# Kernel tuning notes

Hardware: AMD Instinct MI355X
Metric: run time of the kernel (lower is better)

The kernel has to match this reference:

```python
import jax, jax.numpy as jnp
import numpy as np

N_TOKENS = 32768
DIM = 2048
N_EXPERTS = 64
TOP_K = 8
N_GROUP = 8
TOPK_GROUP = 4
ROUTE_SCALE = 2.5
EPS = 1e-20


def setup_inputs() -> dict:
    key = jax.random.key(0)
    k1, k2 = jax.random.split(key)
    hidden_states = jax.random.normal(k1, (N_TOKENS, DIM), dtype=jnp.float32)
    weight = jax.random.normal(k2, (N_EXPERTS, DIM), dtype=jnp.float32) * 0.02
    e_score_correction_bias = jnp.zeros((N_EXPERTS,), dtype=jnp.float32)
    return {"hidden_states": hidden_states, "weight": weight,
            "e_score_correction_bias": e_score_correction_bias}


def reference(hidden_states, weight, e_score_correction_bias):
    # router logits in fp32: [N, E]
    logits = jnp.einsum('nd,ed->ne', hidden_states.astype(jnp.float32),
                        weight.astype(jnp.float32))
    scores = jax.nn.sigmoid(logits)  # score_func == 'sigmoid'

    # --- top-k index selection (no-grad path in torch) ---
    sfc = scores + e_score_correction_bias[None, :]  # [N, E]
    per_group = N_EXPERTS // N_GROUP
    # group score = sum of top-2 scores within each group: [N, G]
    grouped = sfc.reshape(-1, N_GROUP, per_group)
    group_scores = jax.lax.top_k(grouped, 2)[0].sum(axis=-1)
    # pick top `TOPK_GROUP` groups
    _, group_idx = jax.lax.top_k(group_scores, TOPK_GROUP)  # [N, topk_group]
    n = group_scores.shape[0]
    group_mask = jnp.zeros_like(group_scores).at[
        jnp.arange(n)[:, None], group_idx].set(1.0)  # [N, G]
    score_mask = jnp.repeat(group_mask, per_group, axis=1)  # [N, E]
    masked_scores = jnp.where(score_mask > 0, sfc, 0.0)
    _, topk_indices = jax.lax.top_k(masked_scores, TOP_K)  # [N, top_k]

    # gather weights from *unbiased* scores, normalize, scale
    topk_weights = jnp.take_along_axis(scores, topk_indices, axis=1)
    denom = topk_weights.sum(axis=-1, keepdims=True) + EPS
    topk_weights = topk_weights / denom * ROUTE_SCALE
    return topk_indices, topk_weights
```

## Files before the change

### kernel.cpp

```cpp
#include <hip/hip_runtime.h>
#include <math.h>

#define NT 32768
#define DIM 2048
#define NE 64
#define RSCALE 2.5f
#define REPS 1e-20f
#define KC 32
#define NCH (DIM / KC)
#define TOK 64

#define HL_BUF 12288
#define WL_OFF 24576
#define BS_OFF 49152
#define ARENA 49408

typedef __attribute__((ext_vector_type(8))) short short8x;
typedef __attribute__((ext_vector_type(4))) float f32x4;
typedef __attribute__((ext_vector_type(4))) unsigned int uint4x;

#define PACKHI(odd, even) __builtin_amdgcn_perm((odd), (even), 0x07060302u)

__device__ __forceinline__ void decomp4(f32x4 x, unsigned int o[6]) {
    unsigned int u0 = __float_as_uint(x.x), u1 = __float_as_uint(x.y);
    unsigned int u2 = __float_as_uint(x.z), u3 = __float_as_uint(x.w);
    o[0] = PACKHI(u1, u0); o[1] = PACKHI(u3, u2);
    float r0 = x.x - __uint_as_float(u0 & 0xffff0000u);
    float r1 = x.y - __uint_as_float(u1 & 0xffff0000u);
    float r2 = x.z - __uint_as_float(u2 & 0xffff0000u);
    float r3 = x.w - __uint_as_float(u3 & 0xffff0000u);
    unsigned int v0 = __float_as_uint(r0), v1 = __float_as_uint(r1);
    unsigned int v2 = __float_as_uint(r2), v3 = __float_as_uint(r3);
    o[2] = PACKHI(v1, v0); o[3] = PACKHI(v3, v2);
    float s0 = r0 - __uint_as_float(v0 & 0xffff0000u);
    float s1 = r1 - __uint_as_float(v1 & 0xffff0000u);
    float s2 = r2 - __uint_as_float(v2 & 0xffff0000u);
    float s3 = r3 - __uint_as_float(v3 & 0xffff0000u);
    o[4] = PACKHI(__float_as_uint(s1), __float_as_uint(s0));
    o[5] = PACKHI(__float_as_uint(s3), __float_as_uint(s2));
}

__device__ __forceinline__ void decomp8(f32x4 a, f32x4 b,
                                        short8x* f0, short8x* f1, short8x* f2) {
    unsigned int oa[6], ob[6];
    decomp4(a, oa); decomp4(b, ob);
    uint4x t0 = {oa[0], oa[1], ob[0], ob[1]};
    uint4x t1 = {oa[2], oa[3], ob[2], ob[3]};
    uint4x t2 = {oa[4], oa[5], ob[4], ob[5]};
    *f0 = __builtin_bit_cast(short8x, t0);
    *f1 = __builtin_bit_cast(short8x, t1);
    *f2 = __builtin_bit_cast(short8x, t2);
}

#define BARRIER() do { \
    asm volatile("s_waitcnt lgkmcnt(0)" ::: "memory"); \
    __builtin_amdgcn_s_barrier(); \
    __builtin_amdgcn_sched_barrier(0); \
} while (0)

#define STAGE_ISSUE(HA, HB, WA, WB, KOFF) do { \
    HA = *(const f32x4*)(hgsrc + (KOFF));     \
    HB = *(const f32x4*)(hgsrc + (KOFF) + 4); \
    WA = *(const f32x4*)(wgsrc + (KOFF));     \
    WB = *(const f32x4*)(wgsrc + (KOFF) + 4); \
} while (0)

#define STAGE_WRITE(HA, HB, WA, WB, PN) do { \
    short8x f0_, f1_, f2_; \
    decomp8(HA, HB, &f0_, &f1_, &f2_); \
    *(short8x*)(arena + (PN) * HL_BUF + 0 * 4096 + soff) = f0_; \
    *(short8x*)(arena + (PN) * HL_BUF + 1 * 4096 + soff) = f1_; \
    *(short8x*)(arena + (PN) * HL_BUF + 2 * 4096 + soff) = f2_; \
    decomp8(WA, WB, &f0_, &f1_, &f2_); \
    *(short8x*)(arena + WL_OFF + (PN) * HL_BUF + 0 * 4096 + soff) = f0_; \
    *(short8x*)(arena + WL_OFF + (PN) * HL_BUF + 1 * 4096 + soff) = f1_; \
    *(short8x*)(arena + WL_OFF + (PN) * HL_BUF + 2 * 4096 + soff) = f2_; \
} while (0)

#define COMPUTE(P) do { \
    const char* hb = arena + (P) * HL_BUF; \
    const char* wb = arena + WL_OFF + (P) * HL_BUF; \
    short8x a0[2], a1[2], a2[2]; \
    _Pragma("unroll") \
    for (int tt = 0; tt < 2; ++tt) { \
        const int t_ = wr * 32 + tt * 16 + l15; \
        const int ro_ = t_ * 64 + ((g ^ ((t_ >> 1) & 3)) << 4); \
        a0[tt] = *(const short8x*)(hb + 0 * 4096 + ro_); \
        a1[tt] = *(const short8x*)(hb + 1 * 4096 + ro_); \
        a2[tt] = *(const short8x*)(hb + 2 * 4096 + ro_); \
    } \
    _Pragma("unroll") \
    for (int et = 0; et < 2; ++et) { \
        const int e_ = wc * 32 + et * 16 + l15; \
        const int ro_ = e_ * 64 + ((g ^ ((e_ >> 1) & 3)) << 4); \
        short8x b0 = *(const short8x*)(wb + 0 * 4096 + ro_); \
        short8x b1 = *(const short8x*)(wb + 1 * 4096 + ro_); \
        short8x b2 = *(const short8x*)(wb + 2 * 4096 + ro_); \
        _Pragma("unroll") \
        for (int tt = 0; tt < 2; ++tt) { \
            Cm[tt][et] = __builtin_amdgcn_mfma_f32_16x16x32_bf16(a0[tt], b0, Cm[tt][et], 0, 0, 0); \
            Cc[tt][et] = __builtin_amdgcn_mfma_f32_16x16x32_bf16(a1[tt], b0, Cc[tt][et], 0, 0, 0); \
            Cc[tt][et] = __builtin_amdgcn_mfma_f32_16x16x32_bf16(a2[tt], b0, Cc[tt][et], 0, 0, 0); \
            Cc[tt][et] = __builtin_amdgcn_mfma_f32_16x16x32_bf16(a0[tt], b1, Cc[tt][et], 0, 0, 0); \
            Cc[tt][et] = __builtin_amdgcn_mfma_f32_16x16x32_bf16(a1[tt], b1, Cc[tt][et], 0, 0, 0); \
            Cc[tt][et] = __builtin_amdgcn_mfma_f32_16x16x32_bf16(a0[tt], b2, Cc[tt][et], 0, 0, 0); \
        } \
    } \
} while (0)

#define DRAIN do { \
    _Pragma("unroll") \
    for (int tt = 0; tt < 2; ++tt) \
        _Pragma("unroll") \
        for (int et = 0; et < 2; ++et) { \
            _Pragma("unroll") \
            for (int r = 0; r < 4; ++r) \
                md[tt][et][r] += (double)Cm[tt][et][r] + (double)Cc[tt][et][r]; \
            Cm[tt][et] = (f32x4)0.0f; Cc[tt][et] = (f32x4)0.0f; \
        } \
} while (0)

__global__ __launch_bounds__(256, 2) void router_kernel(
    const float* __restrict__ H,
    const float* __restrict__ W,
    const float* __restrict__ B,
    float* __restrict__ out)
{
    __shared__ __align__(16) char arena[ARENA];
    float* bsf = (float*)(arena + BS_OFF);
    float* scf = (float*)(arena);

    const int tid  = threadIdx.x;
    const int lane = tid & 63;
    const int w    = __builtin_amdgcn_readfirstlane(tid >> 6);
    const int l15  = lane & 15, g = lane >> 4;
    const size_t tb = (size_t)blockIdx.x * TOK;

    if (tid < NE) bsf[tid] = B[tid];

    const int srow = tid >> 2;
    const int sq   = tid & 3;
    const float* hgsrc = H + (tb + (size_t)srow) * DIM + sq * 8;
    const float* wgsrc = W + (size_t)srow * DIM + sq * 8;
    const int soff = srow * 64 + ((sq ^ ((srow >> 1) & 3)) << 4);

    const int wr = w & 1, wc = w >> 1;

    f32x4 Cm[2][2], Cc[2][2];
    double md[2][2][4];
    #pragma unroll
    for (int tt = 0; tt < 2; ++tt)
        #pragma unroll
        for (int et = 0; et < 2; ++et) {
            Cm[tt][et] = (f32x4)0.0f; Cc[tt][et] = (f32x4)0.0f;
            #pragma unroll
            for (int r = 0; r < 4; ++r) md[tt][et][r] = 0.0;
        }

    f32x4 hA0, hA1, wA0, wA1, hB0, hB1, wB0, wB1;

    STAGE_ISSUE(hA0, hA1, wA0, wA1, 0);
    STAGE_WRITE(hA0, hA1, wA0, wA1, 0);
    STAGE_ISSUE(hB0, hB1, wB0, wB1, KC);
    BARRIER();

    for (int chb = 0; chb < NCH; chb += 2) {
        if (chb + 2 < NCH) STAGE_ISSUE(hA0, hA1, wA0, wA1, (chb + 2) * KC);
        COMPUTE(0);
        STAGE_WRITE(hB0, hB1, wB0, wB1, 1);
        BARRIER();

        if (chb + 3 < NCH) STAGE_ISSUE(hB0, hB1, wB0, wB1, (chb + 3) * KC);
        COMPUTE(1);
        if (chb + 2 < NCH) STAGE_WRITE(hA0, hA1, wA0, wA1, 0);
        if (((chb + 1) & 7) == 7) DRAIN;
        BARRIER();
    }

    #pragma unroll
    for (int tt = 0; tt < 2; ++tt)
        #pragma unroll
        for (int et = 0; et < 2; ++et)
            #pragma unroll
            for (int r = 0; r < 4; ++r) {
                float logit = (float)md[tt][et][r];
                float s = 1.0f / (1.0f + expf(-logit));
                int t = wr * 32 + tt * 16 + g * 4 + r;
                int e = wc * 32 + et * 16 + l15;
                scf[t * 65 + e] = s;
            }
    __syncthreads();

    if ((tid & 3) == 0) {
        const int t = tid >> 2;
        const float* sc = &scf[t * 65];
        float gs[8];
        #pragma unroll
        for (int gg = 0; gg < 8; ++gg) {
            float m1 = -1e30f, m2 = -1e30f;
            #pragma unroll
            for (int j = 0; j < 8; ++j) {
                float v = sc[gg * 8 + j] + bsf[gg * 8 + j];
                if (v > m1) { m2 = m1; m1 = v; }
                else if (v > m2) { m2 = v; }
            }
            gs[gg] = m1 + m2;
        }
        unsigned gmask = 0;
        for (int i = 0; i < 4; ++i) {
            float best = -1e30f; int bg = 0;
            for (int gg = 0; gg < 8; ++gg)
                if (!((gmask >> gg) & 1u) && gs[gg] > best) { best = gs[gg]; bg = gg; }
            gmask |= 1u << bg;
        }
        unsigned long long picked = 0ull;
        int   idxs[8];
        float wts[8];
        float wsum = 0.0f;
        for (int i = 0; i < 8; ++i) {
            float best = -1e30f; int bi = 0;
            for (int e = 0; e < 64; ++e) {
                if ((picked >> e) & 1ull) continue;
                float v = ((gmask >> (e >> 3)) & 1u) ? (sc[e] + bsf[e]) : 0.0f;
                if (v > best) { best = v; bi = e; }
            }
            picked |= 1ull << bi;
            idxs[i] = bi;
            wts[i] = sc[bi];
            wsum += sc[bi];
        }
        const float scale = RSCALE / (wsum + REPS);
        const size_t token = tb + t;
        #pragma unroll
        for (int i = 0; i < 8; ++i) {
            out[token * 8 + i] = (float)idxs[i];
            out[(size_t)NT * 8 + token * 8 + i] = wts[i] * scale;
        }
    }
}

extern "C" void kernel_launch(void* const* d_in, const int* in_sizes, int n_in,
                              void* d_out, int out_size, void* d_ws, size_t ws_size,
                              hipStream_t stream) {
    (void)in_sizes; (void)n_in; (void)out_size; (void)d_ws; (void)ws_size;
    const float* H = (const float*)d_in[0];
    const float* W = (const float*)d_in[1];
    const float* B = (const float*)d_in[2];
    float* out = (float*)d_out;
    router_kernel<<<dim3(NT / TOK), dim3(256), 0, stream>>>(H, W, B, out);
}
```

Baseline: 131.7 us.

## Split router GEMM along K into four slices with separate top-k reduction kernel

Splits the fp32-emulated GEMM over the hidden dimension into four K-slices on a second grid axis. Partial double-precision logits go to a global scratch buffer, and a new kernel sums them before applying sigmoid and group top-k. Shared memory drops to a single staging buffer with extra barriers so more blocks fit per CU (launch bounds raised to 5). The cost is a 64MB double round trip through global memory, a second kernel launch, and less overlap between loads and compute.

```diff
diff --git a/kernel.cpp b/kernel.cpp
--- a/kernel.cpp
+++ b/kernel.cpp
@@ -7,17 +7,19 @@
 #define RSCALE 2.5f
 #define REPS 1e-20f
 #define KC 32
-#define NCH (DIM / KC)
+#define NSPLIT 4
+#define KSEG (DIM / NSPLIT)
+#define NCHB (KSEG / KC)
 #define TOK 64
 
-#define HL_BUF 12288
-#define WL_OFF 24576
-#define BS_OFF 49152
-#define ARENA 49408
+#define WL_OFF 12288
+#define ARENA 24576
 
 typedef __attribute__((ext_vector_type(8))) short short8x;
 typedef __attribute__((ext_vector_type(4))) float f32x4;
 typedef __attribute__((ext_vector_type(4))) unsigned int uint4x;
+
+__device__ double wsbuf[NSPLIT][NT][NE];
 
 #define PACKHI(odd, even) __builtin_amdgcn_perm((odd), (even), 0x07060302u)
 
@@ -65,21 +67,21 @@
     WB = *(const f32x4*)(wgsrc + (KOFF) + 4); \
 } while (0)
 
-#define STAGE_WRITE(HA, HB, WA, WB, PN) do { \
+#define STAGE_WRITE(HA, HB, WA, WB) do { \
     short8x f0_, f1_, f2_; \
     decomp8(HA, HB, &f0_, &f1_, &f2_); \
-    *(short8x*)(arena + (PN) * HL_BUF + 0 * 4096 + soff) = f0_; \
-    *(short8x*)(arena + (PN) * HL_BUF + 1 * 4096 + soff) = f1_; \
-    *(short8x*)(arena + (PN) * HL_BUF + 2 * 4096 + soff) = f2_; \
+    *(short8x*)(arena + 0 * 4096 + soff) = f0_; \
+    *(short8x*)(arena + 1 * 4096 + soff) = f1_; \
+    *(short8x*)(arena + 2 * 4096 + soff) = f2_; \
     decomp8(WA, WB, &f0_, &f1_, &f2_); \
-    *(short8x*)(arena + WL_OFF + (PN) * HL_BUF + 0 * 4096 + soff) = f0_; \
-    *(short8x*)(arena + WL_OFF + (PN) * HL_BUF + 1 * 4096 + soff) = f1_; \
-    *(short8x*)(arena + WL_OFF + (PN) * HL_BUF + 2 * 4096 + soff) = f2_; \
-} while (0)
-
-#define COMPUTE(P) do { \
-    const char* hb = arena + (P) * HL_BUF; \
-    const char* wb = arena + WL_OFF + (P) * HL_BUF; \
+    *(short8x*)(arena + WL_OFF + 0 * 4096 + soff) = f0_; \
+    *(short8x*)(arena + WL_OFF + 1 * 4096 + soff) = f1_; \
+    *(short8x*)(arena + WL_OFF + 2 * 4096 + soff) = f2_; \
+} while (0)
+
+#define COMPUTE() do { \
+    const char* hb = arena; \
+    const char* wb = arena + WL_OFF; \
     short8x a0[2], a1[2], a2[2]; \
     _Pragma("unroll") \
     for (int tt = 0; tt < 2; ++tt) { \
@@ -120,28 +122,24 @@
         } \
 } while (0)
 
-__global__ __launch_bounds__(256, 2) void router_kernel(
+__global__ __launch_bounds__(256, 5) void router_gemm(
     const float* __restrict__ H,
-    const float* __restrict__ W,
-    const float* __restrict__ B,
-    float* __restrict__ out)
+    const float* __restrict__ W)
 {
     __shared__ __align__(16) char arena[ARENA];
-    float* bsf = (float*)(arena + BS_OFF);
-    float* scf = (float*)(arena);
 
     const int tid  = threadIdx.x;
     const int lane = tid & 63;
     const int w    = __builtin_amdgcn_readfirstlane(tid >> 6);
     const int l15  = lane & 15, g = lane >> 4;
     const size_t tb = (size_t)blockIdx.x * TOK;
-
-    if (tid < NE) bsf[tid] = B[tid];
+    const int split = blockIdx.y;
+    const int kbase = split * KSEG;
 
     const int srow = tid >> 2;
     const int sq   = tid & 3;
-    const float* hgsrc = H + (tb + (size_t)srow) * DIM + sq * 8;
-    const float* wgsrc = W + (size_t)srow * DIM + sq * 8;
+    const float* hgsrc = H + (tb + (size_t)srow) * DIM + kbase + sq * 8;
+    const float* wgsrc = W + (size_t)srow * DIM + kbase + sq * 8;
     const int soff = srow * 64 + ((sq ^ ((srow >> 1) & 3)) << 4);
 
     const int wr = w & 1, wc = w >> 1;
@@ -160,20 +158,22 @@
     f32x4 hA0, hA1, wA0, wA1, hB0, hB1, wB0, wB1;
 
     STAGE_ISSUE(hA0, hA1, wA0, wA1, 0);
-    STAGE_WRITE(hA0, hA1, wA0, wA1, 0);
     STAGE_ISSUE(hB0, hB1, wB0, wB1, KC);
+    STAGE_WRITE(hA0, hA1, wA0, wA1);
     BARRIER();
 
-    for (int chb = 0; chb < NCH; chb += 2) {
-        if (chb + 2 < NCH) STAGE_ISSUE(hA0, hA1, wA0, wA1, (chb + 2) * KC);
-        COMPUTE(0);
-        STAGE_WRITE(hB0, hB1, wB0, wB1, 1);
-        BARRIER();
-
-        if (chb + 3 < NCH) STAGE_ISSUE(hB0, hB1, wB0, wB1, (chb + 3) * KC);
-        COMPUTE(1);
-        if (chb + 2 < NCH) STAGE_WRITE(hA0, hA1, wA0, wA1, 0);
+    for (int chb = 0; chb < NCHB; chb += 2) {
+        COMPUTE();
+        if (chb + 2 < NCHB) STAGE_ISSUE(hA0, hA1, wA0, wA1, (chb + 2) * KC);
+        BARRIER();
+        STAGE_WRITE(hB0, hB1, wB0, wB1);
+        BARRIER();
+
+        COMPUTE();
+        if (chb + 3 < NCHB) STAGE_ISSUE(hB0, hB1, wB0, wB1, (chb + 3) * KC);
         if (((chb + 1) & 7) == 7) DRAIN;
+        BARRIER();
+        if (chb + 2 < NCHB) STAGE_WRITE(hA0, hA1, wA0, wA1);
         BARRIER();
     }
 
@@ -182,13 +182,33 @@
         #pragma unroll
         for (int et = 0; et < 2; ++et)
             #pragma unroll
-            for (int r = 0; r < 4; ++r) {
-                float logit = (float)md[tt][et][r];
-                float s = 1.0f / (1.0f + expf(-logit));
-                int t = wr * 32 + tt * 16 + g * 4 + r;
-                int e = wc * 32 + et * 16 + l15;
-                scf[t * 65 + e] = s;
-            }
+            for (int r = 0; r < 4; ++r)
+                wsbuf[split][tb + wr * 32 + tt * 16 + g * 4 + r]
+                     [wc * 32 + et * 16 + l15] = md[tt][et][r];
+}
+
+__global__ __launch_bounds__(256) void router_topk(
+    const float* __restrict__ B,
+    float* __restrict__ out)
+{
+    __shared__ float scf[TOK * 65];
+    __shared__ float bsf[NE];
+
+    const int tid = threadIdx.x;
+    const size_t tb = (size_t)blockIdx.x * TOK;
+
+    if (tid < NE) bsf[tid] = B[tid];
+
+    const int e  = tid & 63;
+    const int t4 = tid >> 6;
+    #pragma unroll
+    for (int pass = 0; pass < 16; ++pass) {
+        const int t = pass * 4 + t4;
+        const size_t token = tb + t;
+        double m = ((wsbuf[0][token][e] + wsbuf[1][token][e])
+                  + wsbuf[2][token][e]) + wsbuf[3][token][e];
+        scf[t * 65 + e] = 1.0f / (1.0f + expf(-(float)m));
+    }
     __syncthreads();
 
     if ((tid & 3) == 0) {
@@ -219,10 +239,10 @@
         float wsum = 0.0f;
         for (int i = 0; i < 8; ++i) {
             float best = -1e30f; int bi = 0;
-            for (int e = 0; e < 64; ++e) {
-                if ((picked >> e) & 1ull) continue;
-                float v = ((gmask >> (e >> 3)) & 1u) ? (sc[e] + bsf[e]) : 0.0f;
-                if (v > best) { best = v; bi = e; }
+            for (int ee = 0; ee < 64; ++ee) {
+                if ((picked >> ee) & 1ull) continue;
+                float v = ((gmask >> (ee >> 3)) & 1u) ? (sc[ee] + bsf[ee]) : 0.0f;
+                if (v > best) { best = v; bi = ee; }
             }
             picked |= 1ull << bi;
             idxs[i] = bi;
@@ -247,5 +267,6 @@
     const float* W = (const float*)d_in[1];
     const float* B = (const float*)d_in[2];
     float* out = (float*)d_out;
-    router_kernel<<<dim3(NT / TOK), dim3(256), 0, stream>>>(H, W, B, out);
-}
+    router_gemm<<<dim3(NT / TOK, NSPLIT), dim3(256), 0, stream>>>(H, W);
+    router_topk<<<dim3(NT / TOK), dim3(256), 0, stream>>>(B, out);
+}
```

Result: slower. 294.6 us (+123.7%).

## Split K across two wave groups per block with LDS reduction of partial logits

Applied to the files above, without the earlier changes.

Doubles the block to 512 threads, split into two 4-wave groups. Each group handles half of the DIM reduction with its own single-buffered LDS staging area, and the double-precision partial sums are combined through shared memory before the sigmoid and top-k step. The aim is more waves in flight per CU to hide global load latency, and a shorter serial K loop per wave. In exchange the per-group double buffering becomes a single buffer with extra barriers, and a reduction pass through LDS is added.

```diff
diff --git a/kernel.cpp b/kernel.cpp
--- a/kernel.cpp
+++ b/kernel.cpp
@@ -7,13 +7,16 @@
 #define RSCALE 2.5f
 #define REPS 1e-20f
 #define KC 32
-#define NCH (DIM / KC)
+#define NCHG 32
+#define KSEG (NCHG * KC)
 #define TOK 64
 
-#define HL_BUF 12288
-#define WL_OFF 24576
-#define BS_OFF 49152
-#define ARENA 49408
+#define GRP_ARENA 24576
+#define WL_OFF 12288
+#define MD_OFF 0
+#define SC_OFF 32768
+#define BS_OFF 49408
+#define ARENA 49664
 
 typedef __attribute__((ext_vector_type(8))) short short8x;
 typedef __attribute__((ext_vector_type(4))) float f32x4;
@@ -65,21 +68,21 @@
     WB = *(const f32x4*)(wgsrc + (KOFF) + 4); \
 } while (0)
 
-#define STAGE_WRITE(HA, HB, WA, WB, PN) do { \
+#define STAGE_WRITE(HA, HB, WA, WB) do { \
     short8x f0_, f1_, f2_; \
     decomp8(HA, HB, &f0_, &f1_, &f2_); \
-    *(short8x*)(arena + (PN) * HL_BUF + 0 * 4096 + soff) = f0_; \
-    *(short8x*)(arena + (PN) * HL_BUF + 1 * 4096 + soff) = f1_; \
-    *(short8x*)(arena + (PN) * HL_BUF + 2 * 4096 + soff) = f2_; \
+    *(short8x*)(ga + 0 * 4096 + soff) = f0_; \
+    *(short8x*)(ga + 1 * 4096 + soff) = f1_; \
+    *(short8x*)(ga + 2 * 4096 + soff) = f2_; \
     decomp8(WA, WB, &f0_, &f1_, &f2_); \
-    *(short8x*)(arena + WL_OFF + (PN) * HL_BUF + 0 * 4096 + soff) = f0_; \
-    *(short8x*)(arena + WL_OFF + (PN) * HL_BUF + 1 * 4096 + soff) = f1_; \
-    *(short8x*)(arena + WL_OFF + (PN) * HL_BUF + 2 * 4096 + soff) = f2_; \
-} while (0)
-
-#define COMPUTE(P) do { \
-    const char* hb = arena + (P) * HL_BUF; \
-    const char* wb = arena + WL_OFF + (P) * HL_BUF; \
+    *(short8x*)(ga + WL_OFF + 0 * 4096 + soff) = f0_; \
+    *(short8x*)(ga + WL_OFF + 1 * 4096 + soff) = f1_; \
+    *(short8x*)(ga + WL_OFF + 2 * 4096 + soff) = f2_; \
+} while (0)
+
+#define COMPUTE() do { \
+    const char* hb = ga; \
+    const char* wb = ga + WL_OFF; \
     short8x a0[2], a1[2], a2[2]; \
     _Pragma("unroll") \
     for (int tt = 0; tt < 2; ++tt) { \
@@ -120,7 +123,7 @@
         } \
 } while (0)
 
-__global__ __launch_bounds__(256, 2) void router_kernel(
+__global__ __launch_bounds__(512, 4) void router_kernel(
     const float* __restrict__ H,
     const float* __restrict__ W,
     const float* __restrict__ B,
@@ -128,23 +131,30 @@
 {
     __shared__ __align__(16) char arena[ARENA];
     float* bsf = (float*)(arena + BS_OFF);
-    float* scf = (float*)(arena);
+    float* scf = (float*)(arena + SC_OFF);
+    double* mdb = (double*)(arena + MD_OFF);
 
     const int tid  = threadIdx.x;
     const int lane = tid & 63;
     const int w    = __builtin_amdgcn_readfirstlane(tid >> 6);
+    const int grp  = w >> 2;
+    const int wl   = w & 3;
     const int l15  = lane & 15, g = lane >> 4;
     const size_t tb = (size_t)blockIdx.x * TOK;
+    const int kbase = grp * KSEG;
+
+    char* ga = arena + grp * GRP_ARENA;
 
     if (tid < NE) bsf[tid] = B[tid];
 
-    const int srow = tid >> 2;
-    const int sq   = tid & 3;
-    const float* hgsrc = H + (tb + (size_t)srow) * DIM + sq * 8;
-    const float* wgsrc = W + (size_t)srow * DIM + sq * 8;
+    const int gtid = tid & 255;
+    const int srow = gtid >> 2;
+    const int sq   = gtid & 3;
+    const float* hgsrc = H + (tb + (size_t)srow) * DIM + kbase + sq * 8;
+    const float* wgsrc = W + (size_t)srow * DIM + kbase + sq * 8;
     const int soff = srow * 64 + ((sq ^ ((srow >> 1) & 3)) << 4);
 
-    const int wr = w & 1, wc = w >> 1;
+    const int wr = wl & 1, wc = wl >> 1;
 
     f32x4 Cm[2][2], Cc[2][2];
     double md[2][2][4];
@@ -160,38 +170,53 @@
     f32x4 hA0, hA1, wA0, wA1, hB0, hB1, wB0, wB1;
 
     STAGE_ISSUE(hA0, hA1, wA0, wA1, 0);
-    STAGE_WRITE(hA0, hA1, wA0, wA1, 0);
     STAGE_ISSUE(hB0, hB1, wB0, wB1, KC);
+    STAGE_WRITE(hA0, hA1, wA0, wA1);
     BARRIER();
 
-    for (int chb = 0; chb < NCH; chb += 2) {
-        if (chb + 2 < NCH) STAGE_ISSUE(hA0, hA1, wA0, wA1, (chb + 2) * KC);
-        COMPUTE(0);
-        STAGE_WRITE(hB0, hB1, wB0, wB1, 1);
-        BARRIER();
-
-        if (chb + 3 < NCH) STAGE_ISSUE(hB0, hB1, wB0, wB1, (chb + 3) * KC);
-        COMPUTE(1);
-        if (chb + 2 < NCH) STAGE_WRITE(hA0, hA1, wA0, wA1, 0);
+    for (int chb = 0; chb < NCHG; chb += 2) {
+        COMPUTE();
+        if (chb + 2 < NCHG) STAGE_ISSUE(hA0, hA1, wA0, wA1, (chb + 2) * KC);
+        BARRIER();
+        STAGE_WRITE(hB0, hB1, wB0, wB1);
+        BARRIER();
+
+        COMPUTE();
+        if (chb + 3 < NCHG) STAGE_ISSUE(hB0, hB1, wB0, wB1, (chb + 3) * KC);
         if (((chb + 1) & 7) == 7) DRAIN;
         BARRIER();
-    }
-
-    #pragma unroll
-    for (int tt = 0; tt < 2; ++tt)
-        #pragma unroll
-        for (int et = 0; et < 2; ++et)
-            #pragma unroll
-            for (int r = 0; r < 4; ++r) {
-                float logit = (float)md[tt][et][r];
-                float s = 1.0f / (1.0f + expf(-logit));
-                int t = wr * 32 + tt * 16 + g * 4 + r;
-                int e = wc * 32 + et * 16 + l15;
-                scf[t * 65 + e] = s;
-            }
+        if (chb + 2 < NCHG) STAGE_WRITE(hA0, hA1, wA0, wA1);
+        BARRIER();
+    }
+
+    if (grp == 1) {
+        #pragma unroll
+        for (int tt = 0; tt < 2; ++tt)
+            #pragma unroll
+            for (int et = 0; et < 2; ++et)
+                #pragma unroll
+                for (int r = 0; r < 4; ++r)
+                    mdb[((tt * 2 + et) * 4 + r) * 256 + gtid] = md[tt][et][r];
+    }
     __syncthreads();
 
-    if ((tid & 3) == 0) {
+    if (grp == 0) {
+        #pragma unroll
+        for (int tt = 0; tt < 2; ++tt)
+            #pragma unroll
+            for (int et = 0; et < 2; ++et)
+                #pragma unroll
+                for (int r = 0; r < 4; ++r) {
+                    double m = md[tt][et][r] + mdb[((tt * 2 + et) * 4 + r) * 256 + gtid];
+                    float s = 1.0f / (1.0f + expf(-(float)m));
+                    int t = wr * 32 + tt * 16 + g * 4 + r;
+                    int e = wc * 32 + et * 16 + l15;
+                    scf[t * 65 + e] = s;
+                }
+    }
+    __syncthreads();
+
+    if (tid < 256 && (tid & 3) == 0) {
         const int t = tid >> 2;
         const float* sc = &scf[t * 65];
         float gs[8];
@@ -247,5 +272,5 @@
     const float* W = (const float*)d_in[1];
     const float* B = (const float*)d_in[2];
     float* out = (float*)d_out;
-    router_kernel<<<dim3(NT / TOK), dim3(256), 0, stream>>>(H, W, B, out);
-}
+    router_kernel<<<dim3(NT / TOK), dim3(512), 0, stream>>>(H, W, B, out);
+}
```

New measurement: 155.3 us. +17.9%, slower.

## Precompute bf16-split weight image and stream it to LDS with direct loads

Applied to the files above, without the earlier changes.

Adds a prep kernel that converts the router weight into its three-way bf16 split form once, laid out in the swizzled LDS layout, and stores it in a global buffer. The main kernel then copies weight tiles straight into LDS with global_load_lds instead of loading fp32 weights and decomposing them in every block. This removes redundant per-block weight conversion and register traffic. In exchange it adds a second kernel launch, triples the weight bytes read per chunk, and replaces the custom barrier with __syncthreads, which waits on outstanding memory counters.

```diff
diff --git a/kernel.cpp b/kernel.cpp
--- a/kernel.cpp
+++ b/kernel.cpp
@@ -15,9 +15,13 @@
 #define BS_OFF 49152
 #define ARENA 49408
 
+typedef const __attribute__((address_space(1))) void GV;
+typedef __attribute__((address_space(3))) void LV;
 typedef __attribute__((ext_vector_type(8))) short short8x;
 typedef __attribute__((ext_vector_type(4))) float f32x4;
 typedef __attribute__((ext_vector_type(4))) unsigned int uint4x;
+
+__device__ __align__(16) char WImg[NCH][3 * 4096];
 
 #define PACKHI(odd, even) __builtin_amdgcn_perm((odd), (even), 0x07060302u)
 
@@ -52,29 +56,43 @@
     *f2 = __builtin_bit_cast(short8x, t2);
 }
 
-#define BARRIER() do { \
-    asm volatile("s_waitcnt lgkmcnt(0)" ::: "memory"); \
-    __builtin_amdgcn_s_barrier(); \
-    __builtin_amdgcn_sched_barrier(0); \
-} while (0)
-
-#define STAGE_ISSUE(HA, HB, WA, WB, KOFF) do { \
-    HA = *(const f32x4*)(hgsrc + (KOFF));     \
+__global__ void prep_w_kernel(const float* __restrict__ W) {
+    const int ch = blockIdx.x;
+    const int tid = threadIdx.x;
+    const int srow = tid >> 2;
+    const int sq   = tid & 3;
+    const float* src = W + (size_t)srow * DIM + ch * KC + sq * 8;
+    f32x4 lo = *(const f32x4*)src;
+    f32x4 hi = *(const f32x4*)(src + 4);
+    short8x f0, f1, f2;
+    decomp8(lo, hi, &f0, &f1, &f2);
+    const int soff = srow * 64 + ((sq ^ ((srow >> 1) & 3)) << 4);
+    *(short8x*)&WImg[ch][0 * 4096 + soff] = f0;
+    *(short8x*)&WImg[ch][1 * 4096 + soff] = f1;
+    *(short8x*)&WImg[ch][2 * 4096 + soff] = f2;
+}
+
+#define STAGE_ISSUE(HA, HB, KOFF) do { \
+    HA = *(const f32x4*)(hgsrc + (KOFF)); \
     HB = *(const f32x4*)(hgsrc + (KOFF) + 4); \
-    WA = *(const f32x4*)(wgsrc + (KOFF));     \
-    WB = *(const f32x4*)(wgsrc + (KOFF) + 4); \
-} while (0)
-
-#define STAGE_WRITE(HA, HB, WA, WB, PN) do { \
+} while (0)
+
+#define STAGE_WRITE_H(HA, HB, PN) do { \
     short8x f0_, f1_, f2_; \
     decomp8(HA, HB, &f0_, &f1_, &f2_); \
     *(short8x*)(arena + (PN) * HL_BUF + 0 * 4096 + soff) = f0_; \
     *(short8x*)(arena + (PN) * HL_BUF + 1 * 4096 + soff) = f1_; \
     *(short8x*)(arena + (PN) * HL_BUF + 2 * 4096 + soff) = f2_; \
-    decomp8(WA, WB, &f0_, &f1_, &f2_); \
-    *(short8x*)(arena + WL_OFF + (PN) * HL_BUF + 0 * 4096 + soff) = f0_; \
-    *(short8x*)(arena + WL_OFF + (PN) * HL_BUF + 1 * 4096 + soff) = f1_; \
-    *(short8x*)(arena + WL_OFF + (PN) * HL_BUF + 2 * 4096 + soff) = f2_; \
+} while (0)
+
+#define WSTAGE(CHN, PN) do { \
+    const char* ws_ = WImg[(CHN)]; \
+    __builtin_amdgcn_global_load_lds((GV*)(ws_ + 0 * 4096 + wgofs), \
+        (LV*)(arena + WL_OFF + (PN) * HL_BUF + 0 * 4096 + wlofs), 16, 0, 0); \
+    __builtin_amdgcn_global_load_lds((GV*)(ws_ + 1 * 4096 + wgofs), \
+        (LV*)(arena + WL_OFF + (PN) * HL_BUF + 1 * 4096 + wlofs), 16, 0, 0); \
+    __builtin_amdgcn_global_load_lds((GV*)(ws_ + 2 * 4096 + wgofs), \
+        (LV*)(arena + WL_OFF + (PN) * HL_BUF + 2 * 4096 + wlofs), 16, 0, 0); \
 } while (0)
 
 #define COMPUTE(P) do { \
@@ -122,7 +140,6 @@
 
 __global__ __launch_bounds__(256, 2) void router_kernel(
     const float* __restrict__ H,
-    const float* __restrict__ W,
     const float* __restrict__ B,
     float* __restrict__ out)
 {
@@ -141,8 +158,10 @@
     const int srow = tid >> 2;
     const int sq   = tid & 3;
     const float* hgsrc = H + (tb + (size_t)srow) * DIM + sq * 8;
-    const float* wgsrc = W + (size_t)srow * DIM + sq * 8;
     const int soff = srow * 64 + ((sq ^ ((srow >> 1) & 3)) << 4);
+
+    const int wgofs = tid * 16;
+    const int wlofs = w * 1024;
 
     const int wr = w & 1, wc = w >> 1;
 
@@ -157,24 +176,29 @@
             for (int r = 0; r < 4; ++r) md[tt][et][r] = 0.0;
         }
 
-    f32x4 hA0, hA1, wA0, wA1, hB0, hB1, wB0, wB1;
-
-    STAGE_ISSUE(hA0, hA1, wA0, wA1, 0);
-    STAGE_WRITE(hA0, hA1, wA0, wA1, 0);
-    STAGE_ISSUE(hB0, hB1, wB0, wB1, KC);
-    BARRIER();
+    f32x4 hA0, hA1, hB0, hB1;
+
+    WSTAGE(0, 0);
+    STAGE_ISSUE(hA0, hA1, 0);
+    STAGE_WRITE_H(hA0, hA1, 0);
+    STAGE_ISSUE(hB0, hB1, KC);
+    __syncthreads();
 
     for (int chb = 0; chb < NCH; chb += 2) {
-        if (chb + 2 < NCH) STAGE_ISSUE(hA0, hA1, wA0, wA1, (chb + 2) * KC);
+        WSTAGE(chb + 1, 1);
+        if (chb + 2 < NCH) STAGE_ISSUE(hA0, hA1, (chb + 2) * KC);
         COMPUTE(0);
-        STAGE_WRITE(hB0, hB1, wB0, wB1, 1);
-        BARRIER();
-
-        if (chb + 3 < NCH) STAGE_ISSUE(hB0, hB1, wB0, wB1, (chb + 3) * KC);
+        STAGE_WRITE_H(hB0, hB1, 1);
+        __syncthreads();
+
+        if (chb + 2 < NCH) {
+            WSTAGE(chb + 2, 0);
+            STAGE_ISSUE(hB0, hB1, (chb + 3 < NCH) ? (chb + 3) * KC : (chb + 2) * KC);
+        }
         COMPUTE(1);
-        if (chb + 2 < NCH) STAGE_WRITE(hA0, hA1, wA0, wA1, 0);
+        if (chb + 2 < NCH) STAGE_WRITE_H(hA0, hA1, 0);
         if (((chb + 1) & 7) == 7) DRAIN;
-        BARRIER();
+        __syncthreads();
     }
 
     #pragma unroll
@@ -247,5 +271,6 @@
     const float* W = (const float*)d_in[1];
     const float* B = (const float*)d_in[2];
     float* out = (float*)d_out;
-    router_kernel<<<dim3(NT / TOK), dim3(256), 0, stream>>>(H, W, B, out);
-}
+    prep_w_kernel<<<dim3(NCH), dim3(256), 0, stream>>>(W);
+    router_kernel<<<dim3(NT / TOK), dim3(256), 0, stream>>>(H, B, out);
+}
```

Measured after the change: 123.6 us, median of 2. 6.2% less time.
